# Kernel tuning notes

Hardware: AMD Instinct MI355X
Metric: run time of the kernel (lower is better)

The kernel has to match this reference:

```python
import jax, jax.numpy as jnp
import numpy as np

ALPHA = 0.5
TEMP = 0.1
BIG = 1.0e10
THRESH = 1.0e9
NEG = -1.0e10


def setup_inputs() -> dict:
    key = jax.random.key(0)
    k1, k2, k3, k4, k5 = jax.random.split(key, 5)
    B, T, N = 2, 4, 4096
    pred_positions = jax.random.normal(k1, (B, T, N, 3), dtype=jnp.float32)
    target_positions = jax.random.normal(k2, (B, T, N, 3), dtype=jnp.float32)
    is_controller = jax.random.bernoulli(k3, 0.1, (B, N))
    padding_mask = jax.random.bernoulli(k4, 0.95, (B, N))           # True = valid
    visibility_mask = jax.random.bernoulli(k5, 0.9, (B, T, N))      # True = visible
    return {
        "pred_positions": pred_positions,
        "target_positions": target_positions,
        "is_controller": is_controller,
        "padding_mask": padding_mask,
        "visibility_mask": visibility_mask,
    }


def _soft_max(x, temp):
    # differentiable max: sum(x * softmax(x / temp)) with all-invalid rows -> 0
    valid = x > -THRESH
    has_valid = valid.any(axis=-1)
    w = jax.nn.softmax(x / temp, axis=-1)
    r = (x * w).sum(axis=-1)
    return jnp.where(has_valid, r, jnp.zeros_like(r))


def _hybrid_loss(pred, target, mask, alpha, temp):
    # pred, target: (B, T, N, 3); mask: (B, T, N) bool (same mask for pred & target)
    xx = (pred ** 2).sum(-1)[..., :, None]          # (B,T,N,1)
    yy = (target ** 2).sum(-1)[..., None, :]        # (B,T,1,M)
    xy = jnp.einsum('btnd,btmd->btnm', pred, target)
    dist = jnp.maximum(xx + yy - 2.0 * xy, 0.0)     # (B,T,N,M) squared distances

    tgt_m = mask[..., None, :]                      # mask over target axis
    prd_m = mask[..., :, None]                      # mask over pred axis

    d_for_pred = jnp.where(tgt_m, dist, BIG)
    min_p = d_for_pred.min(axis=-1)                 # (B,T,N) min over targets
    d_for_tgt = jnp.where(prd_m, dist, BIG)
    min_t = d_for_tgt.min(axis=-2)                  # (B,T,M) min over preds

    # --- Chamfer ---
    maskf = mask.astype(pred.dtype)
    cd_p = jnp.where(min_p > THRESH, 0.0, min_p) * maskf
    cd_t = jnp.where(min_t > THRESH, 0.0, min_t) * maskf
    num_valid = jnp.maximum(maskf.sum(-1), 1.0)     # (B,T)
    cd = cd_p.sum(-1) / num_valid + cd_t.sum(-1) / num_valid

    # --- Soft Hausdorff ---
    hp = jnp.where(mask, jnp.minimum(min_p, THRESH), NEG)
    ht = jnp.where(mask, jnp.minimum(min_t, THRESH), NEG)
    hd = jnp.maximum(_soft_max(hp, temp), _soft_max(ht, temp))

    cd_loss = cd.mean()                             # mean over (B,T) == per-step mean then /T
    hd_loss = hd.mean()
    total = alpha * cd_loss + (1.0 - alpha) * hd_loss
    return total, cd_loss, hd_loss


def reference(pred_positions, target_positions, is_controller, padding_mask, visibility_mask):
    # object_only=True: particle_mask = ~is_controller & padding_mask
    particle_mask = (~is_controller) & padding_mask          # (B,N)
    mask = particle_mask[:, None, :] & visibility_mask       # (B,T,N)
    total, cd, hd = _hybrid_loss(pred_positions, target_positions, mask, ALPHA, TEMP)
    return total
```

## Files before the change

kernel.cpp:

```cpp
#include <hip/hip_runtime.h>

#define NB 2
#define NT 4
#define NN 4096
#define NBT (NB*NT)
#define TOTAL (NBT*NN)
#define BIGF 1e10f
#define THRESHF 1e9f
#define NEGF (-1e10f)

typedef __attribute__((ext_vector_type(8)))  short s16x8;
typedef __attribute__((ext_vector_type(16))) float f32x16;

__device__ inline unsigned short f2bf(float f) {
    unsigned u = __float_as_uint(f);
    u += 0x7fffu + ((u >> 16) & 1u);
    return (unsigned short)(u >> 16);
}
__device__ inline void split2(float x, unsigned short& hi, unsigned short& lo) {
    hi = f2bf(x);
    float fh = __uint_as_float(((unsigned)hi) << 16);
    lo = f2bf(x - fh);
}
__device__ inline s16x8 mk8(unsigned short a, unsigned short b, unsigned short c, unsigned short d,
                            unsigned short e, unsigned short f, unsigned short g, unsigned short h) {
    return (s16x8){(short)a,(short)b,(short)c,(short)d,(short)e,(short)f,(short)g,(short)h};
}


__global__ __launch_bounds__(256, 4) void min_kernel(
    const float* __restrict__ pred, const float* __restrict__ targ,
    const int* __restrict__ ic, const int* __restrict__ pad, const int* __restrict__ vis,
    unsigned* __restrict__ minp, unsigned* __restrict__ mint,
    float* __restrict__ out)
{
    __shared__ __align__(16) char ldsraw[33792];
    s16x8* ldsB = (s16x8*)ldsraw;

    const int tid  = threadIdx.x;
    const int lane = tid & 63;
    const int w    = tid >> 6;
    const int cc   = blockIdx.x;
    const int rc   = blockIdx.y;
    const int z    = blockIdx.z;
    const int bt   = z >> 1;
    const int dir  = z & 1;
    const int b    = bt >> 2;
    if (cc == 0 && rc == 0 && z == 0 && tid == 0) out[0] = 0.0f;

    const float* __restrict__ rowraw = dir ? targ : pred;
    const float* __restrict__ colraw = dir ? pred : targ;
    unsigned* outp = (dir ? mint : minp) + cc * TOTAL;
    const unsigned short one = 0x3F80;

    #pragma unroll
    for (int r = 0; r < 4; ++r) {
        int nloc = r*256 + tid;
        int n    = cc*1024 + nloc;
        int gi   = bt*NN + n;
        bool m = (ic[b*NN + n] == 0) && (pad[b*NN + n] != 0) && (vis[gi] != 0);
        float bias = m ? 0.0f : BIGF;
        float x = colraw[3*gi], y = colraw[3*gi+1], zc = colraw[3*gi+2];
        unsigned short ux,uy,uz,vx,vy,vz,ch,cl;
        split2(-2.0f*x,ux,vx); split2(-2.0f*y,uy,vy); split2(-2.0f*zc,uz,vz);
        float wn = fmaf(x,x, fmaf(y,y, zc*zc));
        split2(wn + bias, ch, cl);
        int tile = nloc >> 5;
        int c32  = tid & 31;
        ldsB[tile*64 + c32]      = mk8(ux,uy,uz,ux,uy,uz,vx,vy);
        ldsB[tile*64 + 32 + c32] = mk8(vz,ch,cl,one,one,0,0,0);
    }

    const int h  = lane >> 5;
    const int c  = lane & 31;
    const int n0 = rc*256 + w*64;
    s16x8 a[2];
    #pragma unroll
    for (int rt = 0; rt < 2; ++rt) {
        int row = bt*NN + n0 + rt*32 + c;
        float x = rowraw[3*row], y = rowraw[3*row+1], zc = rowraw[3*row+2];
        unsigned short ax,ay,az,bx,by,bz,wh,wl;
        split2(x,ax,bx); split2(y,ay,by); split2(zc,az,bz);
        float wn = fmaf(x,x, fmaf(y,y, zc*zc));
        split2(wn, wh, wl);
        a[rt] = h ? mk8(az,one,one,wh,wl,0,0,0) : mk8(ax,ay,az,bx,by,bz,ax,ay);
    }

    __syncthreads();

    f32x16 zf, mm[2];
    #pragma unroll
    for (int q = 0; q < 16; ++q) { zf[q] = 0.0f; mm[0][q] = 3.4e38f; mm[1][q] = 3.4e38f; }

    #pragma unroll 1
    for (int tp = 0; tp < 16; ++tp) {
        s16x8 b0 = ldsB[tp*128 + lane];
        s16x8 b1 = ldsB[tp*128 + 64 + lane];
        #pragma unroll
        for (int rt = 0; rt < 2; ++rt) {
            f32x16 D0 = __builtin_amdgcn_mfma_f32_32x32x16_bf16(a[rt], b0, zf, 0, 0, 0);
            f32x16 D1 = __builtin_amdgcn_mfma_f32_32x32x16_bf16(a[rt], b1, zf, 0, 0, 0);
            #pragma unroll
            for (int q = 0; q < 16; ++q)
                mm[rt][q] = fminf(fminf(D0[q], D1[q]), mm[rt][q]);
        }
    }

    __syncthreads();
    float* fbuf = (float*)ldsraw;
    const int wbase = w * 2112;
    #pragma unroll
    for (int rt = 0; rt < 2; ++rt) {
        #pragma unroll
        for (int q = 0; q < 16; ++q) {
            int rl = rt*32 + (q & 3) + 8*(q >> 2) + 4*h;
            fbuf[wbase + rl*33 + c] = mm[rt][q];
        }
    }
    const float* rowp = fbuf + wbase + lane*33;
    float v = 3.4e38f;
    #pragma unroll
    for (int k = 0; k < 32; ++k) v = fminf(v, rowp[k]);
    float xv = fmaxf(v, 0.0f);
    unsigned bits = __float_as_uint(xv);
    if (!(xv == xv))         bits = __float_as_uint(BIGF);
    if (bits == 0x80000000u) bits = 0u;
    outp[bt*NN + n0 + lane] = bits;
}

__global__ __launch_bounds__(1024) void finalize_kernel(
    const unsigned* __restrict__ minp, const unsigned* __restrict__ mint,
    const int* __restrict__ ic, const int* __restrict__ pad, const int* __restrict__ vis,
    float* __restrict__ out)
{
    const int bt  = blockIdx.x;
    const int b   = bt >> 2;
    const int tid = threadIdx.x;
    const int S   = TOTAL/4;

    const uint4* pp = (const uint4*)(minp + bt*NN);
    const uint4* tt = (const uint4*)(mint + bt*NN);
    uint4 p0 = pp[tid], p1 = pp[S + tid], p2 = pp[2*S + tid], p3 = pp[3*S + tid];
    uint4 t0 = tt[tid], t1 = tt[S + tid], t2 = tt[2*S + tid], t3 = tt[3*S + tid];
    int4 ic4  = ((const int4*)(ic  + b*NN))[tid];
    int4 pad4 = ((const int4*)(pad + b*NN))[tid];
    int4 vis4 = ((const int4*)(vis + bt*NN))[tid];

    #define MIN4(a,b,c,d) min(min(a,b), min(c,d))
    unsigned pu[4] = { MIN4(p0.x,p1.x,p2.x,p3.x), MIN4(p0.y,p1.y,p2.y,p3.y),
                       MIN4(p0.z,p1.z,p2.z,p3.z), MIN4(p0.w,p1.w,p2.w,p3.w) };
    unsigned tu[4] = { MIN4(t0.x,t1.x,t2.x,t3.x), MIN4(t0.y,t1.y,t2.y,t3.y),
                       MIN4(t0.z,t1.z,t2.z,t3.z), MIN4(t0.w,t1.w,t2.w,t3.w) };
    #undef MIN4
    int icv[4]  = { ic4.x, ic4.y, ic4.z, ic4.w };
    int padv[4] = { pad4.x, pad4.y, pad4.z, pad4.w };
    int visv[4] = { vis4.x, vis4.y, vis4.z, vis4.w };

    float hp[4], ht[4];
    float nv = 0.f, scdp = 0.f, scdt = 0.f, mhp = NEGF, mht = NEGF;
    #pragma unroll
    for (int e = 0; e < 4; ++e) {
        bool m = (icv[e] == 0) && (padv[e] != 0) && (visv[e] != 0);
        float mp = __uint_as_float(pu[e]);
        float mt = __uint_as_float(tu[e]);
        if (!(mp <= 2e10f)) mp = BIGF;
        if (!(mt <= 2e10f)) mt = BIGF;
        float hpv = m ? fminf(mp, THRESHF) : NEGF;
        float htv = m ? fminf(mt, THRESHF) : NEGF;
        hp[e] = hpv; ht[e] = htv;
        if (m) {
            nv += 1.f;
            scdp += (mp > THRESHF) ? 0.f : mp;
            scdt += (mt > THRESHF) ? 0.f : mt;
            mhp = fmaxf(mhp, hpv);
            mht = fmaxf(mht, htv);
        }
    }

    __shared__ float red[16][5];
    const int wid = tid >> 6;
    #pragma unroll
    for (int o = 32; o > 0; o >>= 1) {
        nv   += __shfl_xor(nv, o);
        scdp += __shfl_xor(scdp, o);
        scdt += __shfl_xor(scdt, o);
        mhp   = fmaxf(mhp, __shfl_xor(mhp, o));
        mht   = fmaxf(mht, __shfl_xor(mht, o));
    }
    if ((tid & 63) == 0) {
        red[wid][0] = nv; red[wid][1] = scdp; red[wid][2] = scdt;
        red[wid][3] = mhp; red[wid][4] = mht;
    }
    __syncthreads();
    nv = 0.f; scdp = 0.f; scdt = 0.f; mhp = NEGF; mht = NEGF;
    #pragma unroll
    for (int k = 0; k < 16; ++k) {
        nv += red[k][0]; scdp += red[k][1]; scdt += red[k][2];
        mhp = fmaxf(mhp, red[k][3]); mht = fmaxf(mht, red[k][4]);
    }
    __syncthreads();

    float Zp = 0.f, Sp = 0.f, Zt = 0.f, St = 0.f;
    #pragma unroll
    for (int e = 0; e < 4; ++e) {
        float hpv = hp[e];
        if (hpv > -THRESHF) { float x = __expf((hpv - mhp) * 10.0f); Zp += x; Sp += hpv * x; }
        float htv = ht[e];
        if (htv > -THRESHF) { float x = __expf((htv - mht) * 10.0f); Zt += x; St += htv * x; }
    }
    #pragma unroll
    for (int o = 32; o > 0; o >>= 1) {
        Zp += __shfl_xor(Zp, o);
        Sp += __shfl_xor(Sp, o);
        Zt += __shfl_xor(Zt, o);
        St += __shfl_xor(St, o);
    }
    __shared__ float red2[16][4];
    if ((tid & 63) == 0) {
        red2[wid][0] = Zp; red2[wid][1] = Sp; red2[wid][2] = Zt; red2[wid][3] = St;
    }
    __syncthreads();
    if (tid == 0) {
        Zp = 0.f; Sp = 0.f; Zt = 0.f; St = 0.f;
        #pragma unroll
        for (int k = 0; k < 16; ++k) {
            Zp += red2[k][0]; Sp += red2[k][1]; Zt += red2[k][2]; St += red2[k][3];
        }
        float nvm = fmaxf(nv, 1.f);
        float cd  = scdp / nvm + scdt / nvm;
        float sp  = (nv > 0.f) ? (Sp / Zp) : 0.f;
        float st  = (nv > 0.f) ? (St / Zt) : 0.f;
        float hd  = fmaxf(sp, st);
        atomicAdd(out, (0.5f * cd + 0.5f * hd) * 0.125f);
    }
}

extern "C" void kernel_launch(void* const* d_in, const int* in_sizes, int n_in,
                              void* d_out, int out_size, void* d_ws, size_t ws_size,
                              hipStream_t stream)
{
    const float* pred = (const float*)d_in[0];
    const float* targ = (const float*)d_in[1];
    const int*   ic   = (const int*)d_in[2];
    const int*   pad  = (const int*)d_in[3];
    const int*   vis  = (const int*)d_in[4];
    float* out = (float*)d_out;

    unsigned* minp = (unsigned*)d_ws;
    unsigned* mint = minp + 4*TOTAL;

    dim3 grid(4, 16, 16);
    min_kernel<<<grid, 256, 0, stream>>>(pred, targ, ic, pad, vis, minp, mint, out);
    finalize_kernel<<<NBT, 1024, 0, stream>>>(minp, mint, ic, pad, vis, out);
}
```

Before: 23.56 us.

## Fuse finalize into min kernel using atomicMin and last-block reduction

```diff
diff --git a/kernel.cpp b/kernel.cpp
--- a/kernel.cpp
+++ b/kernel.cpp
@@ -28,13 +28,17 @@
 }
 
 
-__global__ __launch_bounds__(256, 4) void min_kernel(
+
+__global__ __launch_bounds__(256, 4) void hybrid_kernel(
     const float* __restrict__ pred, const float* __restrict__ targ,
     const int* __restrict__ ic, const int* __restrict__ pad, const int* __restrict__ vis,
     unsigned* __restrict__ minp, unsigned* __restrict__ mint,
-    float* __restrict__ out)
+    unsigned* __restrict__ cnt, float* __restrict__ out)
 {
     __shared__ __align__(16) char ldsraw[33792];
+    __shared__ float redA[4][5];
+    __shared__ float redB[4][4];
+    __shared__ int sflag;
     s16x8* ldsB = (s16x8*)ldsraw;
 
     const int tid  = threadIdx.x;
@@ -46,11 +50,10 @@
     const int bt   = z >> 1;
     const int dir  = z & 1;
     const int b    = bt >> 2;
-    if (cc == 0 && rc == 0 && z == 0 && tid == 0) out[0] = 0.0f;
 
     const float* __restrict__ rowraw = dir ? targ : pred;
     const float* __restrict__ colraw = dir ? pred : targ;
-    unsigned* outp = (dir ? mint : minp) + cc * TOTAL;
+    unsigned* outp = dir ? mint : minp;
     const unsigned short one = 0x3F80;
 
     #pragma unroll
@@ -125,60 +128,59 @@
     unsigned bits = __float_as_uint(xv);
     if (!(xv == xv))         bits = __float_as_uint(BIGF);
     if (bits == 0x80000000u) bits = 0u;
-    outp[bt*NN + n0 + lane] = bits;
-}
-
-__global__ __launch_bounds__(1024) void finalize_kernel(
-    const unsigned* __restrict__ minp, const unsigned* __restrict__ mint,
-    const int* __restrict__ ic, const int* __restrict__ pad, const int* __restrict__ vis,
-    float* __restrict__ out)
-{
-    const int bt  = blockIdx.x;
-    const int b   = bt >> 2;
-    const int tid = threadIdx.x;
-    const int S   = TOTAL/4;
-
-    const uint4* pp = (const uint4*)(minp + bt*NN);
-    const uint4* tt = (const uint4*)(mint + bt*NN);
-    uint4 p0 = pp[tid], p1 = pp[S + tid], p2 = pp[2*S + tid], p3 = pp[3*S + tid];
-    uint4 t0 = tt[tid], t1 = tt[S + tid], t2 = tt[2*S + tid], t3 = tt[3*S + tid];
-    int4 ic4  = ((const int4*)(ic  + b*NN))[tid];
-    int4 pad4 = ((const int4*)(pad + b*NN))[tid];
-    int4 vis4 = ((const int4*)(vis + bt*NN))[tid];
-
-    #define MIN4(a,b,c,d) min(min(a,b), min(c,d))
-    unsigned pu[4] = { MIN4(p0.x,p1.x,p2.x,p3.x), MIN4(p0.y,p1.y,p2.y,p3.y),
-                       MIN4(p0.z,p1.z,p2.z,p3.z), MIN4(p0.w,p1.w,p2.w,p3.w) };
-    unsigned tu[4] = { MIN4(t0.x,t1.x,t2.x,t3.x), MIN4(t0.y,t1.y,t2.y,t3.y),
-                       MIN4(t0.z,t1.z,t2.z,t3.z), MIN4(t0.w,t1.w,t2.w,t3.w) };
-    #undef MIN4
-    int icv[4]  = { ic4.x, ic4.y, ic4.z, ic4.w };
-    int padv[4] = { pad4.x, pad4.y, pad4.z, pad4.w };
-    int visv[4] = { vis4.x, vis4.y, vis4.z, vis4.w };
-
-    float hp[4], ht[4];
+    atomicMin(&outp[bt*NN + n0 + lane], bits);
+
+    __syncthreads();
+    if (tid == 0) {
+        __threadfence();
+        unsigned old = atomicAdd(&cnt[bt], 1u);
+        sflag = (old == 127u) ? 1 : 0;
+    }
+    __syncthreads();
+    if (!sflag) return;
+    __threadfence();
+
+    const uint4* mp4 = (const uint4*)(minp + bt*NN);
+    const uint4* mt4 = (const uint4*)(mint + bt*NN);
+    const int4*  ic4p  = (const int4*)(ic  + b*NN);
+    const int4*  pad4p = (const int4*)(pad + b*NN);
+    const int4*  vis4p = (const int4*)(vis + bt*NN);
+
+    float hp[16], ht[16];
     float nv = 0.f, scdp = 0.f, scdt = 0.f, mhp = NEGF, mht = NEGF;
     #pragma unroll
-    for (int e = 0; e < 4; ++e) {
-        bool m = (icv[e] == 0) && (padv[e] != 0) && (visv[e] != 0);
-        float mp = __uint_as_float(pu[e]);
-        float mt = __uint_as_float(tu[e]);
-        if (!(mp <= 2e10f)) mp = BIGF;
-        if (!(mt <= 2e10f)) mt = BIGF;
-        float hpv = m ? fminf(mp, THRESHF) : NEGF;
-        float htv = m ? fminf(mt, THRESHF) : NEGF;
-        hp[e] = hpv; ht[e] = htv;
-        if (m) {
-            nv += 1.f;
-            scdp += (mp > THRESHF) ? 0.f : mp;
-            scdt += (mt > THRESHF) ? 0.f : mt;
-            mhp = fmaxf(mhp, hpv);
-            mht = fmaxf(mht, htv);
+    for (int g = 0; g < 4; ++g) {
+        int i4 = tid + g*256;
+        uint4 p4 = mp4[i4];
+        uint4 t4 = mt4[i4];
+        int4 i4v = ic4p[i4];
+        int4 a4v = pad4p[i4];
+        int4 v4v = vis4p[i4];
+        unsigned pu[4] = { p4.x, p4.y, p4.z, p4.w };
+        unsigned tu[4] = { t4.x, t4.y, t4.z, t4.w };
+        int icv[4]  = { i4v.x, i4v.y, i4v.z, i4v.w };
+        int padv[4] = { a4v.x, a4v.y, a4v.z, a4v.w };
+        int visv[4] = { v4v.x, v4v.y, v4v.z, v4v.w };
+        #pragma unroll
+        for (int e = 0; e < 4; ++e) {
+            bool m = (icv[e] == 0) && (padv[e] != 0) && (visv[e] != 0);
+            float mp = __uint_as_float(pu[e]);
+            float mt = __uint_as_float(tu[e]);
+            if (!(mp <= 2e10f)) mp = BIGF;
+            if (!(mt <= 2e10f)) mt = BIGF;
+            float hpv = m ? fminf(mp, THRESHF) : NEGF;
+            float htv = m ? fminf(mt, THRESHF) : NEGF;
+            hp[g*4+e] = hpv; ht[g*4+e] = htv;
+            if (m) {
+                nv += 1.f;
+                scdp += (mp > THRESHF) ? 0.f : mp;
+                scdt += (mt > THRESHF) ? 0.f : mt;
+                mhp = fmaxf(mhp, hpv);
+                mht = fmaxf(mht, htv);
+            }
         }
     }
 
-    __shared__ float red[16][5];
-    const int wid = tid >> 6;
     #pragma unroll
     for (int o = 32; o > 0; o >>= 1) {
         nv   += __shfl_xor(nv, o);
@@ -187,25 +189,24 @@
         mhp   = fmaxf(mhp, __shfl_xor(mhp, o));
         mht   = fmaxf(mht, __shfl_xor(mht, o));
     }
-    if ((tid & 63) == 0) {
-        red[wid][0] = nv; red[wid][1] = scdp; red[wid][2] = scdt;
-        red[wid][3] = mhp; red[wid][4] = mht;
-    }
-    __syncthreads();
-    nv = 0.f; scdp = 0.f; scdt = 0.f; mhp = NEGF; mht = NEGF;
+    if (lane == 0) {
+        redA[w][0] = nv; redA[w][1] = scdp; redA[w][2] = scdt;
+        redA[w][3] = mhp; redA[w][4] = mht;
+    }
+    __syncthreads();
+    nv   = redA[0][0] + redA[1][0] + redA[2][0] + redA[3][0];
+    scdp = redA[0][1] + redA[1][1] + redA[2][1] + redA[3][1];
+    scdt = redA[0][2] + redA[1][2] + redA[2][2] + redA[3][2];
+    mhp  = fmaxf(fmaxf(redA[0][3], redA[1][3]), fmaxf(redA[2][3], redA[3][3]));
+    mht  = fmaxf(fmaxf(redA[0][4], redA[1][4]), fmaxf(redA[2][4], redA[3][4]));
+    __syncthreads();
+
+    float Zp = 0.f, Sp = 0.f, Zt = 0.f, St = 0.f;
     #pragma unroll
     for (int k = 0; k < 16; ++k) {
-        nv += red[k][0]; scdp += red[k][1]; scdt += red[k][2];
-        mhp = fmaxf(mhp, red[k][3]); mht = fmaxf(mht, red[k][4]);
-    }
-    __syncthreads();
-
-    float Zp = 0.f, Sp = 0.f, Zt = 0.f, St = 0.f;
-    #pragma unroll
-    for (int e = 0; e < 4; ++e) {
-        float hpv = hp[e];
+        float hpv = hp[k];
         if (hpv > -THRESHF) { float x = __expf((hpv - mhp) * 10.0f); Zp += x; Sp += hpv * x; }
-        float htv = ht[e];
+        float htv = ht[k];
         if (htv > -THRESHF) { float x = __expf((htv - mht) * 10.0f); Zt += x; St += htv * x; }
     }
     #pragma unroll
@@ -215,17 +216,15 @@
         Zt += __shfl_xor(Zt, o);
         St += __shfl_xor(St, o);
     }
-    __shared__ float red2[16][4];
-    if ((tid & 63) == 0) {
-        red2[wid][0] = Zp; red2[wid][1] = Sp; red2[wid][2] = Zt; red2[wid][3] = St;
+    if (lane == 0) {
+        redB[w][0] = Zp; redB[w][1] = Sp; redB[w][2] = Zt; redB[w][3] = St;
     }
     __syncthreads();
     if (tid == 0) {
-        Zp = 0.f; Sp = 0.f; Zt = 0.f; St = 0.f;
-        #pragma unroll
-        for (int k = 0; k < 16; ++k) {
-            Zp += red2[k][0]; Sp += red2[k][1]; Zt += red2[k][2]; St += red2[k][3];
-        }
+        Zp = redB[0][0] + redB[1][0] + redB[2][0] + redB[3][0];
+        Sp = redB[0][1] + redB[1][1] + redB[2][1] + redB[3][1];
+        Zt = redB[0][2] + redB[1][2] + redB[2][2] + redB[3][2];
+        St = redB[0][3] + redB[1][3] + redB[2][3] + redB[3][3];
         float nvm = fmaxf(nv, 1.f);
         float cd  = scdp / nvm + scdt / nvm;
         float sp  = (nv > 0.f) ? (Sp / Zp) : 0.f;
@@ -247,9 +246,13 @@
     float* out = (float*)d_out;
 
     unsigned* minp = (unsigned*)d_ws;
-    unsigned* mint = minp + 4*TOTAL;
+    unsigned* mint = minp + TOTAL;
+    unsigned* cnt  = mint + TOTAL;
+
+    hipMemsetAsync(minp, 0xFF, (size_t)2 * TOTAL * 4, stream);
+    hipMemsetAsync(cnt, 0, 16 * 4, stream);
+    hipMemsetAsync(out, 0, 4, stream);
 
     dim3 grid(4, 16, 16);
-    min_kernel<<<grid, 256, 0, stream>>>(pred, targ, ic, pad, vis, minp, mint, out);
-    finalize_kernel<<<NBT, 1024, 0, stream>>>(minp, mint, ic, pad, vis, out);
-}
+    hybrid_kernel<<<grid, 256, 0, stream>>>(pred, targ, ic, pad, vis, minp, mint, cnt, out);
+}
```

Measured after the change: 46.99 us. 99.4% more time.
